# Kernel tuning notes

Measured on AMD Instinct MI355X. Metric: run time of the kernel, lower is better.

The kernel has to match this reference:

```python
import jax, jax.numpy as jnp
import numpy as np

TS = 7           # tile_size
STRIDE = 3       # tile_size - overlap
RATIO = 4
C = 4            # margs.channel
S_LR = 256       # ms side
S_HR = 1024      # margs.test_sidelen
N_ATOMS = 10
TSR = TS * RATIO
STR_R = STRIDE * RATIO
NP_SIDE = (S_LR - TS) // STRIDE + 1   # 84 (pad_size == 0 for this config)
NPATCH = NP_SIDE ** 2                 # 7056


def unfold(x, k, stride):
    # x: [1,C,H,W] -> [1, C*k*k, N]  (channel-major patch layout, same as torch F.unfold)
    p = jax.lax.conv_general_dilated_patches(x, (k, k), (stride, stride), 'VALID')
    return p.reshape(1, p.shape[1], -1)


def fold(p, c, h, w, k, stride):
    # F.fold is the adjoint (overlap-add transpose) of unfold
    _, vjp = jax.vjp(lambda x: unfold(x, k, stride), jnp.zeros((1, c, h, w), p.dtype))
    return vjp(p)[0]


def _gauss(k, sigma):
    ax = np.arange(k) - (k - 1) / 2.0
    g = np.exp(-ax ** 2 / (2.0 * sigma ** 2))
    g = g / g.sum()
    return jnp.asarray(np.outer(g, g), dtype=jnp.float32)


def wald(x, ratio):
    # wald_protocol low-pass: depthwise gaussian blur (MTF approximation)
    k = 4 * ratio + 1
    ker = jnp.broadcast_to(_gauss(k, float(ratio)), (x.shape[1], 1, k, k))
    return jax.lax.conv_general_dilated(x, ker, (1, 1), 'SAME', feature_group_count=x.shape[1])


def setup_inputs() -> dict:
    key = jax.random.key(0)
    ks = jax.random.split(key, 4)
    # histogram-matched PAN high-pass (C channels, matched per band)
    pan_hp = jax.random.normal(ks[0], (1, C, S_HR, S_HR), jnp.float32)
    lr_pan_hp = wald(pan_hp, RATIO)[:, :, 2:-1:4, 2:-1:4]          # [1,C,256,256]
    lr_dict = unfold(lr_pan_hp, TS, STRIDE)[0].T                    # [NPATCH, C*TS^2]
    hr_dict = unfold(pan_hp, TSR, STR_R)[0].T                       # [NPATCH, C*TSR^2]
    ms_hp = 0.1 * jax.random.normal(ks[1], (1, C, S_LR, S_LR), jnp.float32)
    lms = jax.random.normal(ks[2], (1, C, S_HR, S_HR), jnp.float32)
    hrms_hp = 0.1 * jax.random.normal(ks[3], (1, C, S_HR, S_HR), jnp.float32)
    divisor = fold(jnp.ones((1, C * TSR * TSR, NPATCH), jnp.float32), C, S_HR, S_HR, TSR, STR_R)
    divisor = jnp.where(divisor == 0, 1.0, divisor)
    return {"hrms_hp": hrms_hp, "ms_hp": ms_hp, "lms": lms,
            "lr_dict": lr_dict, "hr_dict": hr_dict, "divisor": divisor}


def reference(hrms_hp, ms_hp, lms, lr_dict, hr_dict, divisor):
    N = lr_dict.shape[0]
    hw = TS * TS
    hwr = TSR * TSR
    # residual MS patches: ms_hp - degraded current estimate
    lr_hrms = wald(hrms_hp, RATIO)[:, :, 2:-1:4, 2:-1:4]
    res_ms = unfold(ms_hp - lr_hrms, TS, STRIDE)[0]                 # [C*hw, N]
    res_ms = res_ms.reshape(C, hw, N).transpose(2, 0, 1).reshape(N * C, hw)  # '(n c) hw'
    res = res_ms.reshape(N, C * hw)                                 # 'n (c hw)'
    idx_cols = [jnp.arange(N)]                                      # index[:,0] = arange
    alpha = None
    for i in range(N_ATOMS):
        if i > 0:
            # greedy atom selection: max |<residual, atom>|
            idx_cols.append(jnp.argmax(jnp.abs(res @ lr_dict.T), axis=-1))
        idx = jnp.stack(idx_cols, axis=1)                           # [N, i+1]
        A = lr_dict[idx]                                            # [N, i+1, C*hw]
        A = A.reshape(N, i + 1, C, hw).transpose(0, 2, 3, 1).reshape(N * C, hw, i + 1)
        # batched least squares (min-norm, matches torch.linalg.lstsq)
        alpha = jnp.einsum('bij,bj->bi', jnp.linalg.pinv(A), res_ms)  # [N*C, i+1]
        res = (res_ms - jnp.einsum('bi,bpi->bp', alpha, A)).reshape(N, C * hw)
    idx = jnp.stack(idx_cols, axis=1)                               # [N, N_ATOMS]
    Hd = hr_dict[idx].reshape(N, N_ATOMS, C, hwr).transpose(0, 2, 1, 3).reshape(N * C, N_ATOMS, hwr)
    hr_p = jnp.einsum('bi,bip->bp', alpha, Hd)                      # [N*C, hwr]
    hr_p = hr_p.reshape(N, C, hwr).transpose(1, 2, 0).reshape(1, C * hwr, N)
    hrms_out = fold(hr_p, C, S_HR, S_HR, TSR, STR_R) / (divisor + 1e-8) + hrms_hp
    return hrms_out + lms
```

## Files before the change

### kernel.cpp

```cpp
#include <hip/hip_runtime.h>
#include <math.h>

#define NP    7056
#define NP2   7168
#define NPS   84
#define CCH   4
#define HW    49
#define HWR   784
#define KF    196
#define KSEG  196
#define KC    640
#define NH    20
#define NA    10
#define SLR   256
#define GK    17

typedef _Float16 half8 __attribute__((ext_vector_type(8)));
typedef float f32x4 __attribute__((ext_vector_type(4)));

__global__ void hpass_kernel(const float* __restrict__ hr, float* __restrict__ htmp) {
    __shared__ float g[GK];
    int tid = threadIdx.x;
    if (tid < GK) {
        double s = 0.0, mine = 0.0;
        for (int k = 0; k < GK; k++) {
            double ax = (double)k - 8.0;
            double e = exp(-ax * ax / 32.0);
            s += e;
            if (k == tid) mine = e;
        }
        g[tid] = (float)(mine / s);
    }
    __syncthreads();
    int gid = blockIdx.x * 256 + tid;
    int xs = gid & 255;
    int y  = (gid >> 8) & 1023;
    int c  = gid >> 18;
    const float* row = hr + (size_t)(c * 1024 + y) * 1024;
    int xb = xs * 4 - 6;
    float acc = 0.f;
#pragma unroll
    for (int k = 0; k < GK; k++) {
        int xc = xb + k;
        float v = (xc >= 0 && xc < 1024) ? row[xc] : 0.f;
        acc = fmaf(g[k], v, acc);
    }
    htmp[gid] = acc;
}

__global__ void vpass_kernel(const float* __restrict__ htmp, const float* __restrict__ ms,
                             float* __restrict__ diff) {
    __shared__ float g[GK];
    int tid = threadIdx.x;
    if (tid < GK) {
        double s = 0.0, mine = 0.0;
        for (int k = 0; k < GK; k++) {
            double ax = (double)k - 8.0;
            double e = exp(-ax * ax / 32.0);
            s += e;
            if (k == tid) mine = e;
        }
        g[tid] = (float)(mine / s);
    }
    __syncthreads();
    int gid = blockIdx.x * 256 + tid;
    int xs = gid & 255;
    int ys = (gid >> 8) & 255;
    int c  = gid >> 16;
    int yb = ys * 4 - 6;
    float acc = 0.f;
#pragma unroll
    for (int k = 0; k < GK; k++) {
        int yc = yb + k;
        float v = (yc >= 0 && yc < 1024) ? htmp[(size_t)(c * 1024 + yc) * 256 + xs] : 0.f;
        acc = fmaf(g[k], v, acc);
    }
    diff[gid] = ms[gid] - acc;
}

__global__ void build_y_kernel(const float* __restrict__ diff, float* __restrict__ yb) {
    int gid = blockIdx.x * 256 + threadIdx.x;
    if (gid >= NP * CCH * HW) return;
    int p = gid % HW;
    int b = gid / HW;
    int c = b & 3;
    int n = b >> 2;
    int py = n / NPS, px = n % NPS;
    int dy = p / 7, dx = p % 7;
    yb[gid] = diff[(size_t)(c * SLR + py * 3 + dy) * SLR + px * 3 + dx];
}

__global__ void splitcat_kernel(const float* __restrict__ src, _Float16* __restrict__ Dcat) {
    int gid = blockIdx.x * 256 + threadIdx.x;
    int r = gid / KC, k = gid - r * KC;
    int seg = k / KSEG;
    int ks = k - seg * KSEG;
    float x = (r < NP && seg < 3) ? src[(size_t)r * KF + ks] : 0.f;
    _Float16 hi = (_Float16)x;
    Dcat[gid] = (seg == 1) ? (_Float16)(x - (float)hi) : hi;
}

__global__ void hd16_kernel(const float* __restrict__ hr_dict, _Float16* __restrict__ hd) {
    int gid = blockIdx.x * 256 + threadIdx.x;
    hd[gid] = (_Float16)hr_dict[gid];
}

__device__ __forceinline__ unsigned long long shfl_xor_u64(unsigned long long v, int m) {
    unsigned int lo = (unsigned int)v;
    unsigned int hi = (unsigned int)(v >> 32);
    lo = __shfl_xor(lo, m, 64);
    hi = __shfl_xor(hi, m, 64);
    return ((unsigned long long)hi << 32) | (unsigned long long)lo;
}

__device__ __forceinline__ void gload16(const void* g, void* l) {
    __builtin_amdgcn_global_load_lds((const __attribute__((address_space(1))) void*)(void*)g,
                                     (__attribute__((address_space(3))) void*)l, 16, 0, 0);
}

__global__ __launch_bounds__(512, 4) void mfma_argmax_kernel(
    const _Float16* __restrict__ Rcat, const _Float16* __restrict__ Dcat,
    unsigned long long* __restrict__ keys, int seg) {
    __shared__ __align__(16) _Float16 lds[3 * 12288];
    const int tid = threadIdx.x;
    const int lane = tid & 63;
    const int wave = tid >> 6;
    const int wm = wave >> 1;
    const int wn = wave & 1;

    int b0 = (int)blockIdx.x;
    int xcd = b0 & 7, w = b0 >> 3;
    int bxl = w % 7, by = w / 7;
    int bx = xcd * 7 + bxl;
    const int row0 = by * 256, col0 = bx * 128;

    const int lr = lane & 15, lk = lane >> 4;
    const int xk = (lk ^ ((lr >> 1) & 3)) * 8;
    const int aBase = (wm * 64 + lr) * 32 + xk;
    const int bBase = 8192 + (wn * 64 + lr) * 32 + xk;

    const int srow = wave * 16 + (lane >> 2);
    const int sc = ((lane & 3) ^ ((lane >> 3) & 3)) * 8;
    const _Float16* pA = Rcat + (size_t)(row0 + srow) * KC + sc;
    const _Float16* pB = Dcat + (size_t)(col0 + srow) * KC + sc;
    const int dA1 = wave * 512, dA2 = 4096 + wave * 512, dB = 8192 + wave * 512;

    auto STAGE = [&](int h) {
        int q = (h % 3) * 12288;
        int off = h * 32;
        gload16(pA + off, &lds[q + dA1]);
        gload16(pA + (size_t)128 * KC + off, &lds[q + dA2]);
        gload16(pB + off, &lds[q + dB]);
    };

    f32x4 acc[4][4];
#pragma unroll
    for (int u = 0; u < 4; u++)
#pragma unroll
        for (int v = 0; v < 4; v++) {
            f32x4 zz = {0.f, 0.f, 0.f, 0.f};
            acc[u][v] = zz;
        }

    STAGE(0);
    STAGE(1);
    asm volatile("s_waitcnt vmcnt(3)" ::: "memory");
    __builtin_amdgcn_s_barrier();

    for (int h = 0; h < NH; ++h) {
        const int q = (h % 3) * 12288;
        int hn = h + 2; if (hn > NH - 1) hn = NH - 1;
        STAGE(hn);
        asm volatile("s_waitcnt vmcnt(6)" ::: "memory");
        __builtin_amdgcn_s_barrier();

        half8 aF[4], bF[4];
#pragma unroll
        for (int u = 0; u < 4; ++u)
            aF[u] = *(const half8*)&lds[q + aBase + u * 512];
#pragma unroll
        for (int v = 0; v < 4; ++v)
            bF[v] = *(const half8*)&lds[q + bBase + v * 512];

        __builtin_amdgcn_s_setprio(1);
#pragma unroll
        for (int u = 0; u < 4; ++u)
#pragma unroll
            for (int v = 0; v < 4; ++v)
                acc[u][v] = __builtin_amdgcn_mfma_f32_16x16x32_f16(aF[u], bF[v], acc[u][v], 0, 0, 0);
        __builtin_amdgcn_s_setprio(0);

        asm volatile("s_waitcnt lgkmcnt(0)" ::: "memory");
        __builtin_amdgcn_s_barrier();
    }
    asm volatile("s_waitcnt vmcnt(0)" ::: "memory");

    unsigned long long* kseg = keys + (size_t)seg * NP;
#pragma unroll
    for (int u = 0; u < 4; u++)
#pragma unroll
        for (int j = 0; j < 4; j++) {
            unsigned long long key = 0ull;
#pragma unroll
            for (int v = 0; v < 4; v++) {
                int gc = col0 + wn * 64 + v * 16 + lr;
                if (gc < NP) {
                    unsigned int bits = __float_as_uint(fabsf(acc[u][v][j]));
                    unsigned long long k2 = ((unsigned long long)bits << 32) |
                                            (unsigned long long)(0xFFFFFFFFu - (unsigned int)gc);
                    key = (k2 > key) ? k2 : key;
                }
            }
#pragma unroll
            for (int m = 1; m < 16; m <<= 1) {
                unsigned long long o = shfl_xor_u64(key, m);
                key = (o > key) ? o : key;
            }
            if (lr == 0) {
                int gr = row0 + wm * 64 + u * 16 + lk * 4 + j;
                if (gr < NP) atomicMax(kseg + gr, key);
            }
        }
}

template <int M>
__global__ __launch_bounds__(256) void solve_kernel(
    const float* __restrict__ yb, const float* __restrict__ dict,
    const unsigned long long* __restrict__ keys9,
    int* __restrict__ idxb, float* __restrict__ alphab) {
    int b = blockIdx.x * 256 + threadIdx.x;
    if (b >= NP * CCH) return;
    int n = b >> 2, c = b & 3;

    int newidx = 0;
    if (M >= 2) newidx = (int)(0xFFFFFFFFu -
        (unsigned int)(keys9[(size_t)(M - 2) * NP + n] & 0xFFFFFFFFull));
    if (c == 0) {
        if (M == 1) idxb[n * NA] = n;
        else        idxb[n * NA + (M - 1)] = newidx;
    }

    int id[M];
#pragma unroll
    for (int k = 0; k < M; k++)
        id[k] = (k == 0) ? n : ((M >= 2 && k == M - 1) ? newidx : idxb[n * NA + k]);

    const float* yrow = yb + (size_t)b * HW;
    const int base_c = c * HW;

    constexpr int TRI = M * (M + 1) / 2;
    float G[TRI];
    float rhs[M];
#pragma unroll
    for (int t = 0; t < TRI; t++) G[t] = 0.f;
#pragma unroll
    for (int k = 0; k < M; k++) rhs[k] = 0.f;

#pragma unroll
    for (int p0 = 0; p0 < HW; p0 += 7) {
        float a[M][7];
#pragma unroll
        for (int k = 0; k < M; k++) {
            const float* dr = dict + (size_t)id[k] * KF + base_c + p0;
#pragma unroll
            for (int j = 0; j < 7; j++) a[k][j] = dr[j];
        }
#pragma unroll
        for (int j = 0; j < 7; j++) {
            float yp = yrow[p0 + j];
#pragma unroll
            for (int k = 0; k < M; k++) {
                rhs[k] = fmaf(a[k][j], yp, rhs[k]);
#pragma unroll
                for (int l = 0; l <= k; l++)
                    G[k * (k + 1) / 2 + l] = fmaf(a[k][j], a[l][j], G[k * (k + 1) / 2 + l]);
            }
        }
    }

#pragma unroll
    for (int k = 0; k < M; k++) {
        float s = G[k * (k + 1) / 2 + k];
#pragma unroll
        for (int j = 0; j < k; j++) {
            float l = G[k * (k + 1) / 2 + j];
            s = fmaf(-l, l, s);
        }
        float inv = 1.0f / sqrtf(fmaxf(s, 1e-30f));
        G[k * (k + 1) / 2 + k] = inv;
#pragma unroll
        for (int r = k + 1; r < M; r++) {
            float t = G[r * (r + 1) / 2 + k];
#pragma unroll
            for (int j = 0; j < k; j++)
                t = fmaf(-G[r * (r + 1) / 2 + j], G[k * (k + 1) / 2 + j], t);
            G[r * (r + 1) / 2 + k] = t * inv;
        }
    }
#pragma unroll
    for (int k = 0; k < M; k++) {
        float t = rhs[k];
#pragma unroll
        for (int j = 0; j < k; j++) t = fmaf(-G[k * (k + 1) / 2 + j], rhs[j], t);
        rhs[k] = t * G[k * (k + 1) / 2 + k];
    }
#pragma unroll
    for (int k = M - 1; k >= 0; k--) {
        float t = rhs[k];
#pragma unroll
        for (int j = k + 1; j < M; j++) t = fmaf(-G[j * (j + 1) / 2 + k], rhs[j], t);
        rhs[k] = t * G[k * (k + 1) / 2 + k];
    }

#pragma unroll
    for (int k = 0; k < M; k++) alphab[(size_t)b * NA + k] = rhs[k];
}

template <int M>
__global__ __launch_bounds__(256) void resid_kernel(
    const float* __restrict__ yb, const float* __restrict__ dict,
    const int* __restrict__ idxb, const float* __restrict__ alphab,
    _Float16* __restrict__ Rcat) {
    int gid = blockIdx.x * 256 + threadIdx.x;
    if (gid >= NP * CCH * HW) return;
    int p = gid % HW;
    int b = gid / HW;
    int n = b >> 2, c = b & 3;
    const int base_c = c * HW;
    float s = yb[gid];
#pragma unroll
    for (int k = 0; k < M; k++) {
        int idk = (k == 0) ? n : idxb[n * NA + k];
        s = fmaf(-alphab[(size_t)b * NA + k], dict[(size_t)idk * KF + base_c + p], s);
    }
    _Float16 hi = (_Float16)s;
    _Float16* r0 = Rcat + (size_t)n * KC + base_c;
    r0[p] = hi;
    r0[KSEG + p] = hi;
    r0[2 * KSEG + p] = (_Float16)(s - (float)hi);
}

__global__ __launch_bounds__(256) void recon_kernel(
    const float* __restrict__ alphab, const int* __restrict__ idxb,
    const _Float16* __restrict__ hd, _Float16* __restrict__ hr_p) {
    int n = blockIdx.x;
    int tid = threadIdx.x;
    __shared__ float al[CCH * NA];
    __shared__ int idn[NA];
    if (tid < CCH * NA) al[tid] = alphab[(size_t)n * CCH * NA + tid];
    if (tid < NA) idn[tid] = idxb[n * NA + tid];
    __syncthreads();
    for (int v = tid; v < (CCH * HWR) / 8; v += 256) {
        int c = v / (HWR / 8);
        float s[8] = {0.f, 0.f, 0.f, 0.f, 0.f, 0.f, 0.f, 0.f};
#pragma unroll
        for (int k = 0; k < NA; k++) {
            half8 d = *(const half8*)&hd[(size_t)idn[k] * (CCH * HWR) + v * 8];
            float ak = al[c * NA + k];
#pragma unroll
            for (int e = 0; e < 8; e++) s[e] = fmaf(ak, (float)d[e], s[e]);
        }
        half8 o;
#pragma unroll
        for (int e = 0; e < 8; e++) o[e] = (_Float16)s[e];
        *(half8*)&hr_p[(size_t)n * (CCH * HWR) + v * 8] = o;
    }
}

__global__ __launch_bounds__(256) void fold2_kernel(
    const _Float16* __restrict__ hr_p, const float* __restrict__ divisor,
    const float* __restrict__ hrms, const float* __restrict__ lms,
    float* __restrict__ out) {
    int gid = blockIdx.x * 256 + threadIdx.x;
    int x  = gid & 1023;
    int yy = (gid >> 10) & 1023;
    int c  = gid >> 20;

    int t0 = yy - 27;
    int py0 = (t0 > 0) ? (t0 + 11) / 12 : 0;
    int py1 = min(83, yy / 12);
    int s0 = x - 27;
    int px0 = (s0 > 0) ? (s0 + 11) / 12 : 0;
    int px1 = min(83, x / 12);

    float acc = 0.f;
    for (int py = py0; py <= py1; py++) {
        int qy = yy - py * 12;
        for (int px = px0; px <= px1; px++) {
            int qx = x - px * 12;
            int n = py * NPS + px;
            acc += (float)hr_p[(size_t)n * (CCH * HWR) + c * HWR + qy * 28 + qx];
        }
    }
    out[gid] = acc / (divisor[gid] + 1e-8f) + hrms[gid] + lms[gid];
}

__global__ __launch_bounds__(256) void fold_final_kernel(
    const float* __restrict__ alphab, const int* __restrict__ idxb,
    const float* __restrict__ hr_dict, const float* __restrict__ divisor,
    const float* __restrict__ hrms, const float* __restrict__ lms,
    float* __restrict__ out) {
    int gid = blockIdx.x * 256 + threadIdx.x;
    int x  = gid & 1023;
    int yy = (gid >> 10) & 1023;
    int c  = gid >> 20;
    int t0 = yy - 27;
    int py0 = (t0 > 0) ? (t0 + 11) / 12 : 0;
    int py1 = min(83, yy / 12);
    int s0 = x - 27;
    int px0 = (s0 > 0) ? (s0 + 11) / 12 : 0;
    int px1 = min(83, x / 12);
    float acc = 0.f;
    for (int py = py0; py <= py1; py++) {
        int qy = yy - py * 12;
        for (int px = px0; px <= px1; px++) {
            int qx = x - px * 12;
            int n = py * NPS + px;
            const float* al = alphab + (size_t)(n * CCH + c) * NA;
            const int* idn = idxb + n * NA;
            int q = qy * 28 + qx;
            float s = 0.f;
#pragma unroll
            for (int k = 0; k < NA; k++)
                s = fmaf(al[k], hr_dict[(size_t)idn[k] * (CCH * HWR) + c * HWR + q], s);
            acc += s;
        }
    }
    out[gid] = acc / (divisor[gid] + 1e-8f) + hrms[gid] + lms[gid];
}

extern "C" void kernel_launch(void* const* d_in, const int* in_sizes, int n_in,
                              void* d_out, int out_size, void* d_ws, size_t ws_size,
                              hipStream_t stream) {
    const float* hrms    = (const float*)d_in[0];
    const float* ms      = (const float*)d_in[1];
    const float* lms     = (const float*)d_in[2];
    const float* lr_dict = (const float*)d_in[3];
    const float* hr_dict = (const float*)d_in[4];
    const float* divisor = (const float*)d_in[5];
    float* out = (float*)d_out;

    char* ws = (char*)d_ws;
    size_t off = 0;
    auto alloc = [&](size_t bytes) -> void* {
        void* p = ws + off;
        off += (bytes + 255) & ~(size_t)255;
        return p;
    };
    float* htmp   = (float*)alloc((size_t)4 * 1024 * 256 * 4);
    float* diff   = (float*)alloc((size_t)4 * 256 * 256 * 4);
    float* yb     = (float*)alloc((size_t)NP * CCH * HW * 4);
    float* alphab = (float*)alloc((size_t)NP * CCH * NA * 4);
    int*   idxb   = (int*)alloc((size_t)NP * NA * 4);
    unsigned long long* keys9 = (unsigned long long*)alloc((size_t)NP * 9 * 8);
    _Float16* Dcat = (_Float16*)alloc((size_t)NP2 * KC * 2);
    _Float16* Rcat = (_Float16*)alloc((size_t)NP2 * KC * 2);
    _Float16* hd16 = (_Float16*)alloc((size_t)NP * CCH * HWR * 2);
    _Float16* hr_p = (_Float16*)alloc((size_t)NP * CCH * HWR * 2);
    bool two_stage = (off <= ws_size);

    hpass_kernel<<<4096, 256, 0, stream>>>(hrms, htmp);
    vpass_kernel<<<1024, 256, 0, stream>>>(htmp, ms, diff);
    build_y_kernel<<<(NP * CCH * HW + 255) / 256, 256, 0, stream>>>(diff, yb);
    splitcat_kernel<<<(NP2 * KC) / 256, 256, 0, stream>>>(lr_dict, Dcat);
    hipMemsetAsync(Rcat, 0, (size_t)NP2 * KC * 2, stream);
    hipMemsetAsync(keys9, 0, (size_t)NP * 9 * 8, stream);
    if (two_stage)
        hd16_kernel<<<(NP * CCH * HWR) / 256, 256, 0, stream>>>(hr_dict, hd16);

    int blocks = (NP * CCH + 255) / 256;
    int rblocks = (NP * CCH * HW + 255) / 256;
    for (int i = 0; i < NA; i++) {
        if (i > 0)
            mfma_argmax_kernel<<<1568, 512, 0, stream>>>(Rcat, Dcat, keys9, i - 1);
        switch (i + 1) {
            case 1:  solve_kernel<1><<<blocks, 256, 0, stream>>>(yb, lr_dict, keys9, idxb, alphab);
                     resid_kernel<1><<<rblocks, 256, 0, stream>>>(yb, lr_dict, idxb, alphab, Rcat); break;
            case 2:  solve_kernel<2><<<blocks, 256, 0, stream>>>(yb, lr_dict, keys9, idxb, alphab);
                     resid_kernel<2><<<rblocks, 256, 0, stream>>>(yb, lr_dict, idxb, alphab, Rcat); break;
            case 3:  solve_kernel<3><<<blocks, 256, 0, stream>>>(yb, lr_dict, keys9, idxb, alphab);
                     resid_kernel<3><<<rblocks, 256, 0, stream>>>(yb, lr_dict, idxb, alphab, Rcat); break;
            case 4:  solve_kernel<4><<<blocks, 256, 0, stream>>>(yb, lr_dict, keys9, idxb, alphab);
                     resid_kernel<4><<<rblocks, 256, 0, stream>>>(yb, lr_dict, idxb, alphab, Rcat); break;
            case 5:  solve_kernel<5><<<blocks, 256, 0, stream>>>(yb, lr_dict, keys9, idxb, alphab);
                     resid_kernel<5><<<rblocks, 256, 0, stream>>>(yb, lr_dict, idxb, alphab, Rcat); break;
            case 6:  solve_kernel<6><<<blocks, 256, 0, stream>>>(yb, lr_dict, keys9, idxb, alphab);
                     resid_kernel<6><<<rblocks, 256, 0, stream>>>(yb, lr_dict, idxb, alphab, Rcat); break;
            case 7:  solve_kernel<7><<<blocks, 256, 0, stream>>>(yb, lr_dict, keys9, idxb, alphab);
                     resid_kernel<7><<<rblocks, 256, 0, stream>>>(yb, lr_dict, idxb, alphab, Rcat); break;
            case 8:  solve_kernel<8><<<blocks, 256, 0, stream>>>(yb, lr_dict, keys9, idxb, alphab);
                     resid_kernel<8><<<rblocks, 256, 0, stream>>>(yb, lr_dict, idxb, alphab, Rcat); break;
            case 9:  solve_kernel<9><<<blocks, 256, 0, stream>>>(yb, lr_dict, keys9, idxb, alphab);
                     resid_kernel<9><<<rblocks, 256, 0, stream>>>(yb, lr_dict, idxb, alphab, Rcat); break;
            case 10: solve_kernel<10><<<blocks, 256, 0, stream>>>(yb, lr_dict, keys9, idxb, alphab); break;
        }
    }

    if (two_stage) {
        recon_kernel<<<NP, 256, 0, stream>>>(alphab, idxb, hd16, hr_p);
        fold2_kernel<<<(4 * 1024 * 1024) / 256, 256, 0, stream>>>(hr_p, divisor, hrms, lms, out);
    } else {
        fold_final_kernel<<<(4 * 1024 * 1024) / 256, 256, 0, stream>>>(
            alphab, idxb, hr_dict, divisor, hrms, lms, out);
    }
}
```

Before: 1.344 ms.

## Enlarge argmax GEMM tile to 256x256 with split-phase pipelined staging

Grows the MFMA argmax block tile from 256x128 to 256x256, arranged as 2x4 waves each owning 128x64, and halves the grid to 784 blocks. The main loop is split into two half-phases that interleave A/B global-to-LDS staging with MFMA work, and the block-to-XCD mapping is changed. The goal is more operand reuse per LDS byte and better overlap of loads with compute. In exchange it doubles accumulator registers and LDS per block and lowers occupancy to 2 blocks per CU.

```diff
diff --git a/kernel.cpp b/kernel.cpp
--- a/kernel.cpp
+++ b/kernel.cpp
@@ -10,7 +10,7 @@
 #define KF    196
 #define KSEG  196
 #define KC    640
-#define NH    20
+#define NT    20
 #define NA    10
 #define SLR   256
 #define GK    17
@@ -118,70 +118,86 @@
                                      (__attribute__((address_space(3))) void*)l, 16, 0, 0);
 }
 
-__global__ __launch_bounds__(512, 4) void mfma_argmax_kernel(
+__global__ __launch_bounds__(512, 2) void mfma_argmax_kernel(
     const _Float16* __restrict__ Rcat, const _Float16* __restrict__ Dcat,
     unsigned long long* __restrict__ keys, int seg) {
-    __shared__ __align__(16) _Float16 lds[3 * 12288];
+    __shared__ __align__(16) _Float16 lds[3 * 16384];
     const int tid = threadIdx.x;
     const int lane = tid & 63;
     const int wave = tid >> 6;
-    const int wm = wave >> 1;
-    const int wn = wave & 1;
+    const int wm = wave >> 2;
+    const int wn = wave & 3;
 
     int b0 = (int)blockIdx.x;
     int xcd = b0 & 7, w = b0 >> 3;
-    int bxl = w % 7, by = w / 7;
-    int bx = xcd * 7 + bxl;
-    const int row0 = by * 256, col0 = bx * 128;
+    int by = (xcd >> 1) * 7 + (w % 7);
+    int bx = (xcd & 1) * 14 + (w / 7);
+    const int row0 = by * 256, col0 = bx * 256;
 
     const int lr = lane & 15, lk = lane >> 4;
-    const int xk = (lk ^ ((lr >> 1) & 3)) * 8;
-    const int aBase = (wm * 64 + lr) * 32 + xk;
-    const int bBase = 8192 + (wn * 64 + lr) * 32 + xk;
-
-    const int srow = wave * 16 + (lane >> 2);
-    const int sc = ((lane & 3) ^ ((lane >> 3) & 3)) * 8;
-    const _Float16* pA = Rcat + (size_t)(row0 + srow) * KC + sc;
-    const _Float16* pB = Dcat + (size_t)(col0 + srow) * KC + sc;
-    const int dA1 = wave * 512, dA2 = 4096 + wave * 512, dB = 8192 + wave * 512;
-
-    auto STAGE = [&](int h) {
-        int q = (h % 3) * 12288;
-        int off = h * 32;
-        gload16(pA + off, &lds[q + dA1]);
-        gload16(pA + (size_t)128 * KC + off, &lds[q + dA2]);
-        gload16(pB + off, &lds[q + dB]);
+
+    int aOff[8], bOff[4];
+#pragma unroll
+    for (int u = 0; u < 8; u++) {
+        int r = wm * 128 + u * 16 + lr;
+        aOff[u] = r * 32 + ((lk ^ ((r >> 1) & 3)) * 8);
+    }
+#pragma unroll
+    for (int v = 0; v < 4; v++) {
+        int r = wn * 64 + v * 16 + lr;
+        bOff[v] = 8192 + r * 32 + ((lk ^ ((r >> 1) & 3)) * 8);
+    }
+
+    const int c0 = wave * 128 + lane, c1 = c0 + 64;
+    const int ar0 = c0 >> 2, ax0 = (((c0 & 3) ^ ((ar0 >> 1) & 3)) * 8);
+    const int ar1 = c1 >> 2, ax1 = (((c1 & 3) ^ ((ar1 >> 1) & 3)) * 8);
+    const _Float16* pA0 = Rcat + (size_t)(row0 + ar0) * KC + ax0;
+    const _Float16* pA1 = Rcat + (size_t)(row0 + ar1) * KC + ax1;
+    const _Float16* pB0 = Dcat + (size_t)(col0 + ar0) * KC + ax0;
+    const _Float16* pB1 = Dcat + (size_t)(col0 + ar1) * KC + ax1;
+    const int d0 = c0 * 8, d1 = c1 * 8;
+
+    auto STAGE_A = [&](int h) {
+        int q = (h % 3) * 16384, o = h * 32;
+        gload16(pA0 + o, &lds[q + d0]);
+        gload16(pA1 + o, &lds[q + d1]);
     };
-
-    f32x4 acc[4][4];
-#pragma unroll
-    for (int u = 0; u < 4; u++)
+    auto STAGE_B = [&](int h) {
+        int q = (h % 3) * 16384, o = h * 32;
+        gload16(pB0 + o, &lds[q + 8192 + d0]);
+        gload16(pB1 + o, &lds[q + 8192 + d1]);
+    };
+
+    f32x4 acc[8][4];
+#pragma unroll
+    for (int u = 0; u < 8; u++)
 #pragma unroll
         for (int v = 0; v < 4; v++) {
             f32x4 zz = {0.f, 0.f, 0.f, 0.f};
             acc[u][v] = zz;
         }
 
-    STAGE(0);
-    STAGE(1);
-    asm volatile("s_waitcnt vmcnt(3)" ::: "memory");
+    STAGE_A(0); STAGE_B(0);
+    STAGE_A(1); STAGE_B(1);
+    asm volatile("s_waitcnt vmcnt(4)" ::: "memory");
     __builtin_amdgcn_s_barrier();
 
-    for (int h = 0; h < NH; ++h) {
-        const int q = (h % 3) * 12288;
-        int hn = h + 2; if (hn > NH - 1) hn = NH - 1;
-        STAGE(hn);
-        asm volatile("s_waitcnt vmcnt(6)" ::: "memory");
+    for (int t = 0; t < NT; ++t) {
+        const int q = (t % 3) * 16384;
+        int hn = t + 2; if (hn > NT - 1) hn = NT - 1;
+
+        half8 aF[4], bF[4];
+#pragma unroll
+        for (int v = 0; v < 4; ++v)
+            bF[v] = *(const half8*)&lds[q + bOff[v]];
+#pragma unroll
+        for (int u = 0; u < 4; ++u)
+            aF[u] = *(const half8*)&lds[q + aOff[u]];
+        STAGE_A(hn);
+        asm volatile("" ::: "memory");
         __builtin_amdgcn_s_barrier();
-
-        half8 aF[4], bF[4];
-#pragma unroll
-        for (int u = 0; u < 4; ++u)
-            aF[u] = *(const half8*)&lds[q + aBase + u * 512];
-#pragma unroll
-        for (int v = 0; v < 4; ++v)
-            bF[v] = *(const half8*)&lds[q + bBase + v * 512];
-
+        asm volatile("s_waitcnt lgkmcnt(0)" ::: "memory");
+        __builtin_amdgcn_sched_barrier(0);
         __builtin_amdgcn_s_setprio(1);
 #pragma unroll
         for (int u = 0; u < 4; ++u)
@@ -189,15 +205,33 @@
             for (int v = 0; v < 4; ++v)
                 acc[u][v] = __builtin_amdgcn_mfma_f32_16x16x32_f16(aF[u], bF[v], acc[u][v], 0, 0, 0);
         __builtin_amdgcn_s_setprio(0);
-
+        asm volatile("" ::: "memory");
+        __builtin_amdgcn_s_barrier();
+
+        half8 aG[4];
+#pragma unroll
+        for (int u = 0; u < 4; ++u)
+            aG[u] = *(const half8*)&lds[q + aOff[4 + u]];
+        STAGE_B(hn);
+        asm volatile("s_waitcnt vmcnt(4)" ::: "memory");
+        __builtin_amdgcn_s_barrier();
         asm volatile("s_waitcnt lgkmcnt(0)" ::: "memory");
+        __builtin_amdgcn_sched_barrier(0);
+        __builtin_amdgcn_s_setprio(1);
+#pragma unroll
+        for (int u = 0; u < 4; ++u)
+#pragma unroll
+            for (int v = 0; v < 4; ++v)
+                acc[4 + u][v] = __builtin_amdgcn_mfma_f32_16x16x32_f16(aG[u], bF[v], acc[4 + u][v], 0, 0, 0);
+        __builtin_amdgcn_s_setprio(0);
+        asm volatile("" ::: "memory");
         __builtin_amdgcn_s_barrier();
     }
     asm volatile("s_waitcnt vmcnt(0)" ::: "memory");
 
     unsigned long long* kseg = keys + (size_t)seg * NP;
 #pragma unroll
-    for (int u = 0; u < 4; u++)
+    for (int u = 0; u < 8; u++)
 #pragma unroll
         for (int j = 0; j < 4; j++) {
             unsigned long long key = 0ull;
@@ -217,7 +251,7 @@
                 key = (o > key) ? o : key;
             }
             if (lr == 0) {
-                int gr = row0 + wm * 64 + u * 16 + lk * 4 + j;
+                int gr = row0 + wm * 128 + u * 16 + lk * 4 + j;
                 if (gr < NP) atomicMax(kseg + gr, key);
             }
         }
@@ -472,7 +506,7 @@
     int rblocks = (NP * CCH * HW + 255) / 256;
     for (int i = 0; i < NA; i++) {
         if (i > 0)
-            mfma_argmax_kernel<<<1568, 512, 0, stream>>>(Rcat, Dcat, keys9, i - 1);
+            mfma_argmax_kernel<<<784, 512, 0, stream>>>(Rcat, Dcat, keys9, i - 1);
         switch (i + 1) {
             case 1:  solve_kernel<1><<<blocks, 256, 0, stream>>>(yb, lr_dict, keys9, idxb, alphab);
                      resid_kernel<1><<<rblocks, 256, 0, stream>>>(yb, lr_dict, idxb, alphab, Rcat); break;
```

Result: slower. 1.455 ms (+8.3%).
